# Kernel optimization log

Hardware: AMD Instinct MI355X
Metric: run time of the kernel (lower is better)

Reference implementation:

```python
import jax, jax.numpy as jnp
import numpy as np

EMBED_DIM = 1024
NUM_HEADS = 16
HEAD_DIM = EMBED_DIM // NUM_HEADS
B, S = 2, 2048


def setup_inputs() -> dict:
    key = jax.random.key(0)
    ks = jax.random.split(key, 8)
    std = 1.0 / np.sqrt(EMBED_DIM)
    return {
        "xq": jax.random.normal(ks[0], (B, S, EMBED_DIM), jnp.float32),
        "xk": jax.random.normal(ks[1], (B, S, EMBED_DIM), jnp.float32),
        "xv": jax.random.normal(ks[2], (B, S, EMBED_DIM), jnp.float32),
        "Wq": jax.random.normal(ks[3], (EMBED_DIM, EMBED_DIM), jnp.float32) * std,
        "Wk": jax.random.normal(ks[4], (EMBED_DIM, EMBED_DIM), jnp.float32) * std,
        "Wv": jax.random.normal(ks[5], (EMBED_DIM, EMBED_DIM), jnp.float32) * std,
        "Wo": jax.random.normal(ks[6], (EMBED_DIM, EMBED_DIM), jnp.float32) * std,
        "bo": jnp.zeros((EMBED_DIM,), jnp.float32),
    }


def reference(xq, xk, xv, Wq, Wk, Wv, Wo, bo):
    # nn.Linear(x) = x @ W.T ; then view last dim into (heads, head_dim)
    def proj(x, W):
        y = jnp.einsum('bse,fe->bsf', x, W)
        return y.reshape(x.shape[0], x.shape[1], NUM_HEADS, HEAD_DIM)

    q = proj(xq, Wq)  # [b, m, h, f]
    k = proj(xk, Wk)  # [b, n, h, f]
    v = proj(xv, Wv)  # [b, n, h, f]

    scaling = 1.0 / np.sqrt(HEAD_DIM).astype(np.float32)
    dot = scaling * jnp.einsum('bmhf,bnhf->bhmn', q, k)  # [b, h, m, n]
    attn = jax.nn.softmax(dot, axis=-1)
    out = jnp.einsum('bhmn,bnhf->bmhf', attn, v)  # [b, m, h, f]

    Wo_hf = Wo.reshape(EMBED_DIM, NUM_HEADS, HEAD_DIM)
    return jnp.einsum('bmhf,ehf->bme', out, Wo_hf) + bo
```

## Files before the change

kernel.cpp:

```cpp
#include <hip/hip_runtime.h>
#include <math.h>


#define EMBED 1024
#define SEQ   2048
#define BATCH 2
#define NH    16
#define HD    64

typedef __attribute__((ext_vector_type(8))) short bf16x8;
typedef __attribute__((ext_vector_type(4))) short bf16x4;
typedef __attribute__((ext_vector_type(4))) float f32x4;

#define QSCALE 0.18033688f

__device__ inline unsigned short f2bf(float f) {
  unsigned int u = __builtin_bit_cast(unsigned int, f);
  u += 0x7fffu + ((u >> 16) & 1u);
  return (unsigned short)(u >> 16);
}
__device__ inline float bf2f(unsigned short s) {
  unsigned int u = ((unsigned int)s) << 16;
  return __builtin_bit_cast(float, u);
}

__device__ inline void async_cp16(const void* g, void* l) {
  __builtin_amdgcn_global_load_lds(
      (const __attribute__((address_space(1))) unsigned int*)g,
      (__attribute__((address_space(3))) unsigned int*)l, 16, 0, 0);
}

__global__ void detect_kernel(const unsigned int* __restrict__ xq, int* __restrict__ flag) {
  __shared__ int cnt[256];
  int t = threadIdx.x;
  unsigned int w = xq[t];
  unsigned int e = (w >> 7) & 0xFFu;
  cnt[t] = (e >= 0x70u && e <= 0x8Fu) ? 1 : 0;
  __syncthreads();
  for (int s = 128; s > 0; s >>= 1) {
    if (t < s) cnt[t] += cnt[t + s];
    __syncthreads();
  }
  if (t == 0) *flag = (cnt[0] >= 160) ? 1 : 0;
}

struct PackPtrs {
  const void* src[7];
  unsigned short* dst[7];
};
__global__ __launch_bounds__(256) void pack_all(PackPtrs p, const int* __restrict__ flagp) {
  const bool isbf = (*flagp != 0);
  int ci = blockIdx.x * 256 + threadIdx.x;
  int t, rel;
  if (ci < 1572864) { t = ci / 524288; rel = ci - t * 524288; }
  else { int r = ci - 1572864; int w = r / 131072; t = 3 + w; rel = r - w * 131072; }
  size_t off = (size_t)rel * 8;
  unsigned short* d = p.dst[t] + off;
  if (isbf) {
    *(bf16x8*)d = *(const bf16x8*)((const unsigned short*)p.src[t] + off);
  } else {
    const float* s = (const float*)p.src[t] + off;
    bf16x8 v;
#pragma unroll
    for (int e = 0; e < 8; ++e) v[e] = (short)f2bf(s[e]);
    *(bf16x8*)d = v;
  }
}

struct QkvArgs {
  const unsigned short* A[3];
  const unsigned short* W[3];
  unsigned short* out[3];
};
__global__ __launch_bounds__(256) void gemm_qkv(QkvArgs args) {
  __shared__ __align__(16) unsigned short smem[16640];
  unsigned short* As = smem;
  unsigned short* Bs = smem + 4096;

  const int z = blockIdx.z;
  const unsigned short* A = args.A[z];
  const unsigned short* Bw = args.W[z];
  unsigned short* out = args.out[z];

  const int tid = threadIdx.x, lane = tid & 63, wave = tid >> 6;
  const int wm = wave >> 1, wn = wave & 1;
  const int q = lane >> 4, c = lane & 15;
  const int m0 = blockIdx.x * 128, n0 = blockIdx.y * 128;

  f32x4 acc[4][4];
#pragma unroll
  for (int i = 0; i < 4; ++i)
#pragma unroll
    for (int j = 0; j < 4; ++j) acc[i][j] = (f32x4){0.f, 0.f, 0.f, 0.f};

  for (int k0 = 0; k0 < EMBED; k0 += 32) {
    __syncthreads();
#pragma unroll
    for (int jj = 0; jj < 2; ++jj) {
      int ci = jj * 256 + tid;
      async_cp16(A + (size_t)(m0 + (ci >> 2)) * EMBED + k0 + (ci & 3) * 8,
                 (void*)(As + (jj * 256 + wave * 64) * 8));
      async_cp16(Bw + (size_t)(n0 + (ci >> 2)) * EMBED + k0 + (ci & 3) * 8,
                 (void*)(Bs + (jj * 256 + wave * 64) * 8));
    }
    __syncthreads();

    bf16x8 af[4], bfr[4];
#pragma unroll
    for (int i = 0; i < 4; ++i)
      af[i] = *(const bf16x8*)(As + (wm * 64 + i * 16 + c) * 32 + q * 8);
#pragma unroll
    for (int j = 0; j < 4; ++j)
      bfr[j] = *(const bf16x8*)(Bs + (wn * 64 + j * 16 + c) * 32 + q * 8);
#pragma unroll
    for (int i = 0; i < 4; ++i)
#pragma unroll
      for (int j = 0; j < 4; ++j)
        acc[i][j] = __builtin_amdgcn_mfma_f32_16x16x32_bf16(af[i], bfr[j], acc[i][j], 0, 0, 0);
  }

  if (z < 2) {
    const float sc = (z == 0) ? QSCALE : 1.0f;
#pragma unroll
    for (int i = 0; i < 4; ++i)
#pragma unroll
      for (int j = 0; j < 4; ++j)
#pragma unroll
        for (int r = 0; r < 4; ++r) {
          int m = m0 + wm * 64 + i * 16 + q * 4 + r;
          int col = n0 + wn * 64 + j * 16 + c;
          int b = m >> 11, s = m & 2047, h = col >> 6, d = col & 63;
          out[(size_t)((b * NH + h) * SEQ + s) * HD + d] = f2bf(acc[i][j][r] * sc);
        }
  } else {
    __syncthreads();
#pragma unroll
    for (int i = 0; i < 4; ++i)
#pragma unroll
      for (int j = 0; j < 4; ++j)
#pragma unroll
        for (int r = 0; r < 4; ++r)
          smem[(wm * 64 + i * 16 + q * 4 + r) * 130 + wn * 64 + j * 16 + c] =
              f2bf(acc[i][j][r]);
    __syncthreads();
    int n = tid >> 1;
    int sh = (tid & 1) * 64;
    int b = m0 >> 11, s0l = m0 & 2047;
    int h = blockIdx.y * 2 + (n >> 6), d = n & 63;
    unsigned short* dst = out + (size_t)((b * NH + h) * HD + d) * SEQ + s0l + sh;
#pragma unroll
    for (int g = 0; g < 8; ++g) {
      bf16x8 v;
#pragma unroll
      for (int e = 0; e < 8; ++e) v[e] = (short)smem[(sh + g * 8 + e) * 130 + n];
      *(bf16x8*)(dst + g * 8) = v;
    }
  }
}

__global__ __launch_bounds__(256) void gemm_out(
    const unsigned short* __restrict__ A,
    const unsigned short* __restrict__ Bw,
    const void* __restrict__ bias,
    void* __restrict__ out,
    const int* __restrict__ flagp)
{
  __shared__ __align__(16) unsigned short As[4096];
  __shared__ __align__(16) unsigned short Bs[4096];

  const int tid = threadIdx.x, lane = tid & 63, wave = tid >> 6;
  const int wm = wave >> 1, wn = wave & 1;
  const int q = lane >> 4, c = lane & 15;
  const int m0 = blockIdx.x * 128, n0 = blockIdx.y * 128;

  f32x4 acc[4][4];
#pragma unroll
  for (int i = 0; i < 4; ++i)
#pragma unroll
    for (int j = 0; j < 4; ++j) acc[i][j] = (f32x4){0.f, 0.f, 0.f, 0.f};

  for (int k0 = 0; k0 < EMBED; k0 += 32) {
    __syncthreads();
#pragma unroll
    for (int jj = 0; jj < 2; ++jj) {
      int ci = jj * 256 + tid;
      async_cp16(A + (size_t)(m0 + (ci >> 2)) * EMBED + k0 + (ci & 3) * 8,
                 (void*)(As + (jj * 256 + wave * 64) * 8));
      async_cp16(Bw + (size_t)(n0 + (ci >> 2)) * EMBED + k0 + (ci & 3) * 8,
                 (void*)(Bs + (jj * 256 + wave * 64) * 8));
    }
    __syncthreads();

    bf16x8 af[4], bfr[4];
#pragma unroll
    for (int i = 0; i < 4; ++i)
      af[i] = *(const bf16x8*)(As + (wm * 64 + i * 16 + c) * 32 + q * 8);
#pragma unroll
    for (int j = 0; j < 4; ++j)
      bfr[j] = *(const bf16x8*)(Bs + (wn * 64 + j * 16 + c) * 32 + q * 8);
#pragma unroll
    for (int i = 0; i < 4; ++i)
#pragma unroll
      for (int j = 0; j < 4; ++j)
        acc[i][j] = __builtin_amdgcn_mfma_f32_16x16x32_bf16(af[i], bfr[j], acc[i][j], 0, 0, 0);
  }

  const bool isbf = (*flagp != 0);
#pragma unroll
  for (int i = 0; i < 4; ++i)
#pragma unroll
    for (int j = 0; j < 4; ++j)
#pragma unroll
      for (int r = 0; r < 4; ++r) {
        int m = m0 + wm * 64 + i * 16 + q * 4 + r;
        int col = n0 + wn * 64 + j * 16 + c;
        float v = acc[i][j][r];
        v += isbf ? bf2f(((const unsigned short*)bias)[col]) : ((const float*)bias)[col];
        if (isnan(v)) v = 777.0f;
        if (isbf) ((unsigned short*)out)[(size_t)m * EMBED + col] = f2bf(v);
        else      ((float*)out)[(size_t)m * EMBED + col] = v;
      }
}

__global__ __launch_bounds__(256) void attn_kernel(
    const unsigned short* __restrict__ Qb,
    const unsigned short* __restrict__ Kb,
    const unsigned short* __restrict__ Vtb,
    unsigned short* __restrict__ Ob)
{
  __shared__ __align__(16) unsigned short Kt[2][64][72];
  __shared__ __align__(16) unsigned short Vs[2][64][72];

  const int tid = threadIdx.x;
  const int lane = tid & 63;
  const int wave = tid >> 6;
  const int q = lane >> 4, c = lane & 15;
  const int b = blockIdx.z, h = blockIdx.y;
  const int q0 = blockIdx.x * 128 + wave * 32;

  const unsigned short* Qh = Qb + ((size_t)(b * NH + h) * SEQ) * HD;
  const unsigned short* Kh = Kb + ((size_t)(b * NH + h) * SEQ) * HD;
  const unsigned short* Vh = Vtb + ((size_t)(b * NH + h) * HD) * SEQ;

  bf16x8 qflA = *(const bf16x8*)(Qh + (q0 + c) * HD + q * 8);
  bf16x8 qfhA = *(const bf16x8*)(Qh + (q0 + c) * HD + 32 + q * 8);
  bf16x8 qflB = *(const bf16x8*)(Qh + (q0 + 16 + c) * HD + q * 8);
  bf16x8 qfhB = *(const bf16x8*)(Qh + (q0 + 16 + c) * HD + 32 + q * 8);

  f32x4 oA[4], oB[4];
#pragma unroll
  for (int t = 0; t < 4; ++t) { oA[t] = (f32x4){0.f,0.f,0.f,0.f}; oB[t] = (f32x4){0.f,0.f,0.f,0.f}; }
  f32x4 lA = (f32x4){0.f,0.f,0.f,0.f}, lB = (f32x4){0.f,0.f,0.f,0.f};

  bf16x8 ones;
#pragma unroll
  for (int e = 0; e < 8; ++e) ones[e] = (short)0x3F80;

  const int r0 = tid >> 3;
  const int ch0 = (tid & 7) * 8;

  bf16x8 kr0, kr1, vr0, vr1;
  kr0 = *(const bf16x8*)(Kh + (size_t)r0 * HD + ch0);
  kr1 = *(const bf16x8*)(Kh + (size_t)(32 + r0) * HD + ch0);
  vr0 = *(const bf16x8*)(Vh + (size_t)r0 * SEQ + ch0);
  vr1 = *(const bf16x8*)(Vh + (size_t)(32 + r0) * SEQ + ch0);
  *(bf16x8*)(&Kt[0][r0][ch0]) = kr0;
  *(bf16x8*)(&Kt[0][32 + r0][ch0]) = kr1;
  *(bf16x8*)(&Vs[0][r0][ch0]) = vr0;
  *(bf16x8*)(&Vs[0][32 + r0][ch0]) = vr1;

  for (int kt = 0; kt < SEQ / 64; ++kt) {
    const int p = kt & 1;
    __syncthreads();
    if (kt + 1 < SEQ / 64) {
      kr0 = *(const bf16x8*)(Kh + (size_t)((kt + 1) * 64 + r0) * HD + ch0);
      kr1 = *(const bf16x8*)(Kh + (size_t)((kt + 1) * 64 + 32 + r0) * HD + ch0);
      vr0 = *(const bf16x8*)(Vh + (size_t)r0 * SEQ + (kt + 1) * 64 + ch0);
      vr1 = *(const bf16x8*)(Vh + (size_t)(32 + r0) * SEQ + (kt + 1) * 64 + ch0);
    }

#pragma unroll
    for (int g = 0; g < 2; ++g) {
      bf16x4 pkA[2], pkB[2];
#pragma unroll
      for (int s2 = 0; s2 < 2; ++s2) {
        const int s = g * 2 + s2;
        bf16x8 k0f = *(const bf16x8*)(&Kt[p][s * 16 + c][q * 8]);
        bf16x8 k1f = *(const bf16x8*)(&Kt[p][s * 16 + c][32 + q * 8]);
        f32x4 zA = {0.f, 0.f, 0.f, 0.f};
        f32x4 zB = {0.f, 0.f, 0.f, 0.f};
        zA = __builtin_amdgcn_mfma_f32_16x16x32_bf16(k0f, qflA, zA, 0, 0, 0);
        zA = __builtin_amdgcn_mfma_f32_16x16x32_bf16(k1f, qfhA, zA, 0, 0, 0);
        zB = __builtin_amdgcn_mfma_f32_16x16x32_bf16(k0f, qflB, zB, 0, 0, 0);
        zB = __builtin_amdgcn_mfma_f32_16x16x32_bf16(k1f, qfhB, zB, 0, 0, 0);
#pragma unroll
        for (int r = 0; r < 4; ++r) {
          float pvA = __builtin_amdgcn_exp2f(zA[r]);
          float pvB = __builtin_amdgcn_exp2f(zB[r]);
          pkA[s2][r] = (short)(__builtin_bit_cast(unsigned int, pvA) >> 16);
          pkB[s2][r] = (short)(__builtin_bit_cast(unsigned int, pvB) >> 16);
        }
      }
      bf16x8 pfA, pfB;
#pragma unroll
      for (int e = 0; e < 4; ++e) {
        pfA[e] = pkA[0][e]; pfA[4 + e] = pkA[1][e];
        pfB[e] = pkB[0][e]; pfB[4 + e] = pkB[1][e];
      }
      __builtin_amdgcn_s_setprio(1);
      lA = __builtin_amdgcn_mfma_f32_16x16x32_bf16(pfA, ones, lA, 0, 0, 0);
      lB = __builtin_amdgcn_mfma_f32_16x16x32_bf16(pfB, ones, lB, 0, 0, 0);
#pragma unroll
      for (int t = 0; t < 4; ++t) {
        bf16x4 v0 = *(const bf16x4*)(&Vs[p][t * 16 + c][g * 32 + q * 4]);
        bf16x4 v1 = *(const bf16x4*)(&Vs[p][t * 16 + c][g * 32 + 16 + q * 4]);
        bf16x8 vf;
#pragma unroll
        for (int e = 0; e < 4; ++e) { vf[e] = v0[e]; vf[4 + e] = v1[e]; }
        oA[t] = __builtin_amdgcn_mfma_f32_16x16x32_bf16(pfA, vf, oA[t], 0, 0, 0);
        oB[t] = __builtin_amdgcn_mfma_f32_16x16x32_bf16(pfB, vf, oB[t], 0, 0, 0);
      }
      __builtin_amdgcn_s_setprio(0);
    }

    if (kt + 1 < SEQ / 64) {
      *(bf16x8*)(&Kt[1 - p][r0][ch0]) = kr0;
      *(bf16x8*)(&Kt[1 - p][32 + r0][ch0]) = kr1;
      *(bf16x8*)(&Vs[1 - p][r0][ch0]) = vr0;
      *(bf16x8*)(&Vs[1 - p][32 + r0][ch0]) = vr1;
    }
  }

  float invA[4], invB[4];
#pragma unroll
  for (int r = 0; r < 4; ++r) { invA[r] = 1.0f / lA[r]; invB[r] = 1.0f / lB[r]; }
#pragma unroll
  for (int t = 0; t < 4; ++t)
#pragma unroll
    for (int r = 0; r < 4; ++r) {
      int col = h * HD + t * 16 + c;
      int srowA = q0 + q * 4 + r;
      float vA = oA[t][r] * invA[r];
      if (isnan(vA)) vA = 77.0f;
      Ob[((size_t)(b * SEQ + srowA)) * EMBED + col] = f2bf(vA);
      int srowB = q0 + 16 + q * 4 + r;
      float vB = oB[t][r] * invB[r];
      if (isnan(vB)) vB = 77.0f;
      Ob[((size_t)(b * SEQ + srowB)) * EMBED + col] = f2bf(vB);
    }
}

__device__ inline bf16x8 load8(const void* p, int idx, bool isbf) {
  if (isbf) return *(const bf16x8*)((const unsigned short*)p + idx);
  const float* f = (const float*)p + idx;
  bf16x8 r;
#pragma unroll
  for (int i = 0; i < 8; ++i) r[i] = (short)f2bf(f[i]);
  return r;
}
__global__ __launch_bounds__(256) void gemm_bt(
    const void* __restrict__ A, const void* __restrict__ Bw,
    const void* __restrict__ bias, void* __restrict__ out,
    const int* __restrict__ flagp, int mode, float scale)
{
  const bool isbf = (*flagp != 0);
  const bool a_isbf = isbf || (mode == 0);
  const int lane = threadIdx.x & 63;
  const int wave = threadIdx.x >> 6;
  const int tile = blockIdx.x * 4 + wave;
  const int mt = tile >> 4, nt = tile & 15;
  const int q = lane >> 4, c = lane & 15;
  const int m0 = mt * 16, n0 = nt * 64;

  f32x4 acc[4];
#pragma unroll
  for (int t = 0; t < 4; ++t) acc[t] = (f32x4){0.f, 0.f, 0.f, 0.f};

  for (int k0 = 0; k0 < EMBED; k0 += 32) {
    bf16x8 a = load8(A, (m0 + c) * EMBED + k0 + q * 8, a_isbf);
#pragma unroll
    for (int t = 0; t < 4; ++t) {
      bf16x8 b = load8(Bw, (n0 + t * 16 + c) * EMBED + k0 + q * 8, isbf);
      acc[t] = __builtin_amdgcn_mfma_f32_16x16x32_bf16(a, b, acc[t], 0, 0, 0);
    }
  }
#pragma unroll
  for (int t = 0; t < 4; ++t)
#pragma unroll
    for (int r = 0; r < 4; ++r) {
      float v = acc[t][r] * scale;
      int row = m0 + q * 4 + r, col = n0 + t * 16 + c;
      if (mode == 0) {
        v += isbf ? bf2f(((const unsigned short*)bias)[col]) : ((const float*)bias)[col];
        if (isbf) ((unsigned short*)out)[row * EMBED + col] = f2bf(v);
        else      ((float*)out)[row * EMBED + col] = v;
      } else {
        int b = row >> 11, s = row & 2047, h = col >> 6, d = col & 63;
        if (mode == 1) ((unsigned short*)out)[(((b * NH + h) * SEQ) + s) * HD + d] = f2bf(v);
        else           ((unsigned short*)out)[(((b * NH + h) * HD) + d) * SEQ + s] = f2bf(v);
      }
    }
}

extern "C" void kernel_launch(void* const* d_in, const int* in_sizes, int n_in,
                              void* d_out, int out_size, void* d_ws, size_t ws_size,
                              hipStream_t stream) {
  const void* xq = d_in[0]; const void* xk = d_in[1]; const void* xv = d_in[2];
  const void* Wq = d_in[3]; const void* Wk = d_in[4]; const void* Wv = d_in[5];
  const void* Wo = d_in[6]; const void* bo = d_in[7];

  const size_t NEL = (size_t)BATCH * SEQ * EMBED;
  const size_t WEL = (size_t)EMBED * EMBED;
  unsigned short* base = (unsigned short*)d_ws;

  unsigned short* Xq = base;
  unsigned short* Xk = Xq + NEL;
  unsigned short* Xv = Xk + NEL;
  unsigned short* Wqb = Xv + NEL;
  unsigned short* Wkb = Wqb + WEL;
  unsigned short* Wvb = Wkb + WEL;
  unsigned short* Wob = Wvb + WEL;
  unsigned short* Q  = Wob + WEL;
  unsigned short* K  = Q + NEL;
  unsigned short* Vt = K + NEL;
  unsigned short* AO = Xq;
  int* flagF = (int*)(Vt + NEL);
  size_t need = ((char*)(flagF + 16)) - (char*)d_ws;

  if (ws_size >= need) {
    detect_kernel<<<1, 256, 0, stream>>>((const unsigned int*)xq, flagF);
    PackPtrs pp;
    pp.src[0] = xq; pp.src[1] = xk; pp.src[2] = xv;
    pp.src[3] = Wq; pp.src[4] = Wk; pp.src[5] = Wv; pp.src[6] = Wo;
    pp.dst[0] = Xq; pp.dst[1] = Xk; pp.dst[2] = Xv;
    pp.dst[3] = Wqb; pp.dst[4] = Wkb; pp.dst[5] = Wvb; pp.dst[6] = Wob;
    pack_all<<<8192, 256, 0, stream>>>(pp, flagF);

    QkvArgs qa;
    qa.A[0] = Xq; qa.A[1] = Xk; qa.A[2] = Xv;
    qa.W[0] = Wqb; qa.W[1] = Wkb; qa.W[2] = Wvb;
    qa.out[0] = Q; qa.out[1] = K; qa.out[2] = Vt;
    gemm_qkv<<<dim3(32, 8, 3), 256, 0, stream>>>(qa);
    attn_kernel<<<dim3(SEQ / 128, NH, BATCH), 256, 0, stream>>>(Q, K, Vt, AO);
    gemm_out<<<dim3(32, 8), 256, 0, stream>>>(AO, Wob, bo, d_out, flagF);
  } else {
    unsigned short* Qf  = base;
    unsigned short* Kf  = Qf + NEL;
    unsigned short* Vtf = Kf + NEL;
    unsigned short* AOf = Vtf + NEL;
    int* flag = (int*)(AOf + NEL);
    detect_kernel<<<1, 256, 0, stream>>>((const unsigned int*)xq, flag);
    dim3 gblk(1024, 1, 1);
    gemm_bt<<<gblk, 256, 0, stream>>>(xq, Wq, nullptr, Qf, flag, 1, QSCALE);
    gemm_bt<<<gblk, 256, 0, stream>>>(xk, Wk, nullptr, Kf, flag, 1, 1.0f);
    gemm_bt<<<gblk, 256, 0, stream>>>(xv, Wv, nullptr, Vtf, flag, 2, 1.0f);
    attn_kernel<<<dim3(SEQ / 128, NH, BATCH), 256, 0, stream>>>(Qf, Kf, Vtf, AOf);
    gemm_bt<<<gblk, 256, 0, stream>>>(AOf, Wo, bo, d_out, flag, 0, 1.0f);
  }
}
```

Measured before the change: 239.8 us.

## Double-buffer LDS tiles in QKV and output projection GEMMs

Both projection GEMMs now keep two shared-memory buffers for the A and B tiles. Each iteration issues the async copy of the next K-slice into the idle buffer before running MFMAs on the current one, with a single barrier per iteration instead of two. This is meant to hide global-to-LDS load latency behind matrix compute. In exchange it doubles the tile LDS footprint of the output GEMM, which may reduce occupancy, and it relies on the barrier also waiting for the outstanding async copies.

```diff
diff --git a/kernel.cpp b/kernel.cpp
--- a/kernel.cpp
+++ b/kernel.cpp
@@ -74,8 +74,6 @@
 };
 __global__ __launch_bounds__(256) void gemm_qkv(QkvArgs args) {
   __shared__ __align__(16) unsigned short smem[16640];
-  unsigned short* As = smem;
-  unsigned short* Bs = smem + 4096;
 
   const int z = blockIdx.z;
   const unsigned short* A = args.A[z];
@@ -93,30 +91,38 @@
 #pragma unroll
     for (int j = 0; j < 4; ++j) acc[i][j] = (f32x4){0.f, 0.f, 0.f, 0.f};
 
-  for (int k0 = 0; k0 < EMBED; k0 += 32) {
-    __syncthreads();
+  auto STAGE = [&](int buf, int k0) {
 #pragma unroll
     for (int jj = 0; jj < 2; ++jj) {
       int ci = jj * 256 + tid;
       async_cp16(A + (size_t)(m0 + (ci >> 2)) * EMBED + k0 + (ci & 3) * 8,
-                 (void*)(As + (jj * 256 + wave * 64) * 8));
+                 (void*)(smem + buf * 8192 + (jj * 256 + wave * 64) * 8));
       async_cp16(Bw + (size_t)(n0 + (ci >> 2)) * EMBED + k0 + (ci & 3) * 8,
-                 (void*)(Bs + (jj * 256 + wave * 64) * 8));
-    }
-    __syncthreads();
+                 (void*)(smem + buf * 8192 + 4096 + (jj * 256 + wave * 64) * 8));
+    }
+  };
+
+  STAGE(0, 0);
+  __syncthreads();
+  for (int kt = 0; kt < EMBED / 32; ++kt) {
+    const int p = kt & 1;
+    if (kt + 1 < EMBED / 32) STAGE(1 - p, (kt + 1) * 32);
+    const unsigned short* Ab = smem + p * 8192;
+    const unsigned short* Bb = smem + p * 8192 + 4096;
 
     bf16x8 af[4], bfr[4];
 #pragma unroll
     for (int i = 0; i < 4; ++i)
-      af[i] = *(const bf16x8*)(As + (wm * 64 + i * 16 + c) * 32 + q * 8);
+      af[i] = *(const bf16x8*)(Ab + (wm * 64 + i * 16 + c) * 32 + q * 8);
 #pragma unroll
     for (int j = 0; j < 4; ++j)
-      bfr[j] = *(const bf16x8*)(Bs + (wn * 64 + j * 16 + c) * 32 + q * 8);
+      bfr[j] = *(const bf16x8*)(Bb + (wn * 64 + j * 16 + c) * 32 + q * 8);
 #pragma unroll
     for (int i = 0; i < 4; ++i)
 #pragma unroll
       for (int j = 0; j < 4; ++j)
         acc[i][j] = __builtin_amdgcn_mfma_f32_16x16x32_bf16(af[i], bfr[j], acc[i][j], 0, 0, 0);
+    __syncthreads();
   }
 
   if (z < 2) {
@@ -165,8 +171,7 @@
     void* __restrict__ out,
     const int* __restrict__ flagp)
 {
-  __shared__ __align__(16) unsigned short As[4096];
-  __shared__ __align__(16) unsigned short Bs[4096];
+  __shared__ __align__(16) unsigned short smem[16384];
 
   const int tid = threadIdx.x, lane = tid & 63, wave = tid >> 6;
   const int wm = wave >> 1, wn = wave & 1;
@@ -179,30 +184,38 @@
 #pragma unroll
     for (int j = 0; j < 4; ++j) acc[i][j] = (f32x4){0.f, 0.f, 0.f, 0.f};
 
-  for (int k0 = 0; k0 < EMBED; k0 += 32) {
-    __syncthreads();
+  auto STAGE = [&](int buf, int k0) {
 #pragma unroll
     for (int jj = 0; jj < 2; ++jj) {
       int ci = jj * 256 + tid;
       async_cp16(A + (size_t)(m0 + (ci >> 2)) * EMBED + k0 + (ci & 3) * 8,
-                 (void*)(As + (jj * 256 + wave * 64) * 8));
+                 (void*)(smem + buf * 8192 + (jj * 256 + wave * 64) * 8));
       async_cp16(Bw + (size_t)(n0 + (ci >> 2)) * EMBED + k0 + (ci & 3) * 8,
-                 (void*)(Bs + (jj * 256 + wave * 64) * 8));
-    }
-    __syncthreads();
+                 (void*)(smem + buf * 8192 + 4096 + (jj * 256 + wave * 64) * 8));
+    }
+  };
+
+  STAGE(0, 0);
+  __syncthreads();
+  for (int kt = 0; kt < EMBED / 32; ++kt) {
+    const int p = kt & 1;
+    if (kt + 1 < EMBED / 32) STAGE(1 - p, (kt + 1) * 32);
+    const unsigned short* Ab = smem + p * 8192;
+    const unsigned short* Bb = smem + p * 8192 + 4096;
 
     bf16x8 af[4], bfr[4];
 #pragma unroll
     for (int i = 0; i < 4; ++i)
-      af[i] = *(const bf16x8*)(As + (wm * 64 + i * 16 + c) * 32 + q * 8);
+      af[i] = *(const bf16x8*)(Ab + (wm * 64 + i * 16 + c) * 32 + q * 8);
 #pragma unroll
     for (int j = 0; j < 4; ++j)
-      bfr[j] = *(const bf16x8*)(Bs + (wn * 64 + j * 16 + c) * 32 + q * 8);
+      bfr[j] = *(const bf16x8*)(Bb + (wn * 64 + j * 16 + c) * 32 + q * 8);
 #pragma unroll
     for (int i = 0; i < 4; ++i)
 #pragma unroll
       for (int j = 0; j < 4; ++j)
         acc[i][j] = __builtin_amdgcn_mfma_f32_16x16x32_bf16(af[i], bfr[j], acc[i][j], 0, 0, 0);
+    __syncthreads();
   }
 
   const bool isbf = (*flagp != 0);
```

After: 228.3 us. 1.05x faster.
